# Performance work log

Measured on AMD Instinct MI355X. Metric: run time of the kernel, lower is better.

Reference implementation:

```python
import jax, jax.numpy as jnp
import numpy as np


def _pairwise_l2(x):
    # x: [N, D] -> [N, N] Euclidean distances, matching (x_i - x_j).norm(dim=-1)
    sq = jnp.sum(x * x, axis=-1)                      # [N]
    sqd = sq[:, None] + sq[None, :] - 2.0 * (x @ x.T)  # [N, N] squared distances
    sqd = jnp.maximum(sqd, 0.0)
    # safe sqrt: zero distance (diagonal) -> 0 with zero gradient, matching
    # torch's norm subgradient at 0
    pos = sqd > 0.0
    return jnp.where(pos, jnp.sqrt(jnp.where(pos, sqd, 1.0)), 0.0)


def setup_inputs() -> dict:
    key = jax.random.key(0)
    data = jax.random.normal(key, (8192, 256), dtype=jnp.float32)
    return {"data": data}


def reference(data) -> jnp.ndarray:
    x = data.reshape(data.shape[0], -1)               # [N, D]
    dist = _pairwise_l2(x)                            # [N, N]
    denom = jax.lax.stop_gradient(jnp.sum(dist, axis=1, keepdims=True))
    return dist / denom
```

## Files before the change

kernel.cpp:

```cpp
#include <hip/hip_runtime.h>
#include <stdint.h>

#define NN 8192
#define DD 256

typedef __attribute__((ext_vector_type(8))) short short8;
typedef __attribute__((ext_vector_type(4))) float f32x4;

typedef const uint32_t __attribute__((address_space(1)))* gbl_ptr_t;
typedef uint32_t __attribute__((address_space(3)))* lds_ptr_t;

__device__ __forceinline__ void gl_lds16(const void* g, const void* l) {
    __builtin_amdgcn_global_load_lds((gbl_ptr_t)(uintptr_t)g,
                                     (lds_ptr_t)(uintptr_t)l, 16, 0, 0);
}

__device__ __forceinline__ unsigned short f32_to_bf16(float f) {
    uint32_t u = __float_as_uint(f);
    u += 0x7fff + ((u >> 16) & 1);
    return (unsigned short)(u >> 16);
}
__device__ __forceinline__ float bf16_to_f32(unsigned short h) {
    return __uint_as_float(((uint32_t)h) << 16);
}

__global__ void prep_kernel(const float* __restrict__ x,
                            unsigned short* __restrict__ hi,
                            unsigned short* __restrict__ lo,
                            float* __restrict__ sq,
                            float* __restrict__ denom) {
    const int r = blockIdx.x;
    const int t = threadIdx.x;
    float v = x[(size_t)r * DD + t];
    unsigned short h = f32_to_bf16(v);
    unsigned short l = f32_to_bf16(v - bf16_to_f32(h));
    int csw = (t & ~63) | ((((t >> 3) & 7) ^ (r & 7)) << 3) | (t & 7);
    hi[(size_t)r * DD + csw] = h;
    lo[(size_t)r * DD + csw] = l;

    float s = v * v;
    #pragma unroll
    for (int m = 32; m >= 1; m >>= 1) s += __shfl_xor(s, m, 64);
    __shared__ float ws[4];
    if ((t & 63) == 0) ws[t >> 6] = s;
    __syncthreads();
    if (t == 0) {
        sq[r] = ws[0] + ws[1] + ws[2] + ws[3];
        denom[r] = 0.0f;
    }
}

#define DIST_KLOOP()                                                          \
    for (int kt = 0; kt < 4; ++kt) {                                          \
        _Pragma("unroll")                                                     \
        for (int c = 0; c < 4; ++c) {                                         \
            int lin  = c * 256 + tid;                                         \
            int row  = lin >> 3;                                              \
            int col8 = lin & 7;                                               \
            size_t goffA = (size_t)(row0 + row) * DD + kt * 64 + col8 * 8;    \
            size_t goffB = (size_t)(col0 + row) * DD + kt * 64 + col8 * 8;    \
            size_t lbyte = (size_t)(c * 256 + wid * 64) * 16;                 \
            gl_lds16(hi + goffA, (const char*)ldsAhi + lbyte);                \
            gl_lds16(lo + goffA, (const char*)ldsAlo + lbyte);                \
            gl_lds16(hi + goffB, (const char*)ldsBhi + lbyte);                \
            gl_lds16(lo + goffB, (const char*)ldsBlo + lbyte);                \
        }                                                                     \
        __syncthreads();                                                      \
        _Pragma("unroll")                                                     \
        for (int ks = 0; ks < 2; ++ks) {                                      \
            short8 ah[4], al[4], bh[4], bl[4];                                \
            _Pragma("unroll")                                                 \
            for (int fm = 0; fm < 4; ++fm) {                                  \
                int row = wm * 64 + fm * 16 + l15;                            \
                int cb  = (ks * 64 + lk * 16) ^ ((row & 7) << 4);             \
                int off = row * 64 + (cb >> 1);                               \
                ah[fm] = *(const short8*)(ldsAhi + off);                      \
                al[fm] = *(const short8*)(ldsAlo + off);                      \
            }                                                                 \
            _Pragma("unroll")                                                 \
            for (int fn = 0; fn < 4; ++fn) {                                  \
                int row = wn * 64 + fn * 16 + l15;                            \
                int cb  = (ks * 64 + lk * 16) ^ ((row & 7) << 4);             \
                int off = row * 64 + (cb >> 1);                               \
                bh[fn] = *(const short8*)(ldsBhi + off);                      \
                bl[fn] = *(const short8*)(ldsBlo + off);                      \
            }                                                                 \
            _Pragma("unroll")                                                 \
            for (int fm = 0; fm < 4; ++fm)                                    \
                _Pragma("unroll")                                             \
                for (int fn = 0; fn < 4; ++fn) {                              \
                    acc[fm][fn] = __builtin_amdgcn_mfma_f32_16x16x32_bf16(    \
                        ah[fm], bh[fn], acc[fm][fn], 0, 0, 0);                \
                    acc[fm][fn] = __builtin_amdgcn_mfma_f32_16x16x32_bf16(    \
                        ah[fm], bl[fn], acc[fm][fn], 0, 0, 0);                \
                    acc[fm][fn] = __builtin_amdgcn_mfma_f32_16x16x32_bf16(    \
                        al[fm], bh[fn], acc[fm][fn], 0, 0, 0);                \
                }                                                             \
        }                                                                     \
        __syncthreads();                                                      \
    }

#define DIST_PROLOG()                                                         \
    const int tid  = threadIdx.x;                                             \
    const int lane = tid & 63;                                                \
    const int wid  = tid >> 6;                                                \
    const int wm = wid >> 1, wn = wid & 1;                                    \
    const int l15 = lane & 15, lk = lane >> 4;                                \
    int t = blockIdx.x, bi = 0;                                               \
    while (t >= 64 - bi) { t -= 64 - bi; ++bi; }                              \
    const int bj = bi + t;                                                    \
    const int row0 = bi * 128;                                                \
    const int col0 = bj * 128;                                                \
    const bool offdiag = (bj > bi);                                           \
    f32x4 acc[4][4];                                                          \
    _Pragma("unroll")                                                         \
    for (int a = 0; a < 4; ++a)                                               \
        _Pragma("unroll")                                                     \
        for (int b = 0; b < 4; ++b) acc[a][b] = (f32x4){0.f, 0.f, 0.f, 0.f};  \
    float rsq[4][4], csq[4];                                                  \
    _Pragma("unroll")                                                         \
    for (int fm = 0; fm < 4; ++fm)                                            \
        _Pragma("unroll")                                                     \
        for (int r = 0; r < 4; ++r)                                           \
            rsq[fm][r] = sq[row0 + wm * 64 + fm * 16 + lk * 4 + r];           \
    _Pragma("unroll")                                                         \
    for (int fn = 0; fn < 4; ++fn)                                            \
        csq[fn] = sq[col0 + wn * 64 + fn * 16 + l15];

__launch_bounds__(256, 2)
__global__ void sum_kernel(const unsigned short* __restrict__ hi,
                           const unsigned short* __restrict__ lo,
                           const float* __restrict__ sq,
                           float* __restrict__ denom) {
    __shared__ __align__(16) unsigned short lds[4 * 128 * 64];
    unsigned short* ldsAhi = lds;
    unsigned short* ldsAlo = lds + 8192;
    unsigned short* ldsBhi = lds + 16384;
    unsigned short* ldsBlo = lds + 24576;

    DIST_PROLOG()
    DIST_KLOOP()

    float rp[4][4], cp[4];
    #pragma unroll
    for (int a = 0; a < 4; ++a) {
        cp[a] = 0.f;
        #pragma unroll
        for (int b = 0; b < 4; ++b) rp[a][b] = 0.f;
    }
    #pragma unroll
    for (int fm = 0; fm < 4; ++fm)
        #pragma unroll
        for (int fn = 0; fn < 4; ++fn)
            #pragma unroll
            for (int r = 0; r < 4; ++r) {
                float sqd = rsq[fm][r] + csq[fn] - 2.0f * acc[fm][fn][r];
                float d = sqrtf(fmaxf(sqd, 0.0f));
                rp[fm][r] += d;
                if (offdiag) cp[fn] += d;
            }

    #pragma unroll
    for (int fm = 0; fm < 4; ++fm)
        #pragma unroll
        for (int r = 0; r < 4; ++r) {
            float v = rp[fm][r];
            v += __shfl_xor(v, 1, 64);
            v += __shfl_xor(v, 2, 64);
            v += __shfl_xor(v, 4, 64);
            v += __shfl_xor(v, 8, 64);
            if (l15 == 0)
                atomicAdd(&denom[row0 + wm * 64 + fm * 16 + lk * 4 + r], v);
        }
    if (offdiag) {
        #pragma unroll
        for (int fn = 0; fn < 4; ++fn) {
            float v = cp[fn];
            v += __shfl_xor(v, 16, 64);
            v += __shfl_xor(v, 32, 64);
            if (lane < 16)
                atomicAdd(&denom[col0 + wn * 64 + fn * 16 + l15], v);
        }
    }
}

__global__ void inv_kernel(float* __restrict__ denom) {
    int i = blockIdx.x * 256 + threadIdx.x;
    if (i < NN) denom[i] = 1.0f / denom[i];
}

__launch_bounds__(256, 2)
__global__ void write_kernel(const unsigned short* __restrict__ hi,
                             const unsigned short* __restrict__ lo,
                             const float* __restrict__ sq,
                             const float* __restrict__ inv,
                             float* __restrict__ out) {
    __shared__ __align__(16) unsigned short lds[4 * 128 * 64];
    unsigned short* ldsAhi = lds;
    unsigned short* ldsAlo = lds + 8192;
    unsigned short* ldsBhi = lds + 16384;
    unsigned short* ldsBlo = lds + 24576;

    DIST_PROLOG()

    float rinv[4][4];
    #pragma unroll
    for (int fm = 0; fm < 4; ++fm)
        #pragma unroll
        for (int r = 0; r < 4; ++r)
            rinv[fm][r] = inv[row0 + wm * 64 + fm * 16 + lk * 4 + r];

    DIST_KLOOP()

    float* ldsT = reinterpret_cast<float*>(lds);

    #pragma unroll
    for (int fm = 0; fm < 4; ++fm)
        #pragma unroll
        for (int fn = 0; fn < 4; ++fn)
            #pragma unroll
            for (int r = 0; r < 4; ++r) {
                float sqd = rsq[fm][r] + csq[fn] - 2.0f * acc[fm][fn][r];
                float d = sqrtf(fmaxf(sqd, 0.0f));
                int lr = wm * 64 + fm * 16 + lk * 4 + r;
                int lc = wn * 64 + fn * 16 + l15;
                out[(size_t)(row0 + lr) * NN + col0 + lc] = d * rinv[fm][r];
                if (offdiag)
                    ldsT[lc * 128 + (lr ^ ((lc & 31) ^ ((lc & 4) << 2)))] = d;
            }

    if (offdiag) {
        __syncthreads();
        #pragma unroll
        for (int it = 0; it < 64; ++it) {
            int idx = it * 256 + tid;
            int c  = idx >> 7;
            int r_ = idx & 127;
            float d = ldsT[c * 128 + (r_ ^ ((c & 31) ^ ((c & 4) << 2)))];
            out[(size_t)(col0 + c) * NN + row0 + r_] = d * inv[col0 + c];
        }
    }
}

extern "C" void kernel_launch(void* const* d_in, const int* in_sizes, int n_in,
                              void* d_out, int out_size, void* d_ws, size_t ws_size,
                              hipStream_t stream) {
    const float* x = (const float*)d_in[0];
    float* out = (float*)d_out;
    char* ws = (char*)d_ws;
    unsigned short* hi = (unsigned short*)ws;
    unsigned short* lo = (unsigned short*)(ws + (size_t)NN * DD * 2);
    float* sq    = (float*)(ws + (size_t)NN * DD * 4);
    float* denom = (float*)(ws + (size_t)NN * DD * 4 + NN * 4);

    prep_kernel<<<NN, 256, 0, stream>>>(x, hi, lo, sq, denom);
    sum_kernel<<<2080, 256, 0, stream>>>(hi, lo, sq, denom);
    inv_kernel<<<32, 256, 0, stream>>>(denom);
    write_kernel<<<2080, 256, 0, stream>>>(hi, lo, sq, denom, out);
}
```

Before: 425.6 us.

## Double-buffer K-loop with async LDS prefetch and remap block-to-tile order

Replaces the single-buffered 4-step K loop (64-wide K tiles, loads then barrier) with an 8-step loop over 32-wide K tiles that alternates between two LDS buffers. The next-but-one stage's global-to-LDS loads are issued while the current stage computes, and explicit vmcnt/lgkmcnt waits and barriers control the hand-off. The XOR swizzle in the prep kernel and the LDS reads change to match the new 32-column tile layout. The block index is also permuted across groups of 8 to change which tiles run together, and a sync is added before the write kernel reuses LDS for the transpose. The hand-written waitcnt values are fragile and must exactly match the number of outstanding loads per stage.

```diff
diff --git a/kernel.cpp b/kernel.cpp
--- a/kernel.cpp
+++ b/kernel.cpp
@@ -23,6 +23,14 @@
 __device__ __forceinline__ float bf16_to_f32(unsigned short h) {
     return __uint_as_float(((uint32_t)h) << 16);
 }
+
+#define WAITVM8()  do { asm volatile("s_waitcnt vmcnt(8)" ::: "memory"); \
+                        __builtin_amdgcn_sched_barrier(0); } while (0)
+#define WAITVM0()  do { asm volatile("s_waitcnt vmcnt(0)" ::: "memory"); \
+                        __builtin_amdgcn_sched_barrier(0); } while (0)
+#define WAITLG0()  do { asm volatile("s_waitcnt lgkmcnt(0)" ::: "memory"); \
+                        __builtin_amdgcn_sched_barrier(0); } while (0)
+#define BAR()      __builtin_amdgcn_s_barrier()
 
 __global__ void prep_kernel(const float* __restrict__ x,
                             unsigned short* __restrict__ hi,
@@ -34,7 +42,7 @@
     float v = x[(size_t)r * DD + t];
     unsigned short h = f32_to_bf16(v);
     unsigned short l = f32_to_bf16(v - bf16_to_f32(h));
-    int csw = (t & ~63) | ((((t >> 3) & 7) ^ (r & 7)) << 3) | (t & 7);
+    int csw = (t & ~31) | ((((t >> 3) & 3) ^ (r & 3)) << 3) | (t & 7);
     hi[(size_t)r * DD + csw] = h;
     lo[(size_t)r * DD + csw] = l;
 
@@ -50,54 +58,62 @@
     }
 }
 
+#define STAGE(st, p) do {                                                     \
+    _Pragma("unroll")                                                         \
+    for (int c = 0; c < 2; ++c) {                                             \
+        int lin  = c * 256 + tid;                                             \
+        int row  = lin >> 2;                                                  \
+        int col8 = lin & 3;                                                   \
+        size_t gA = (size_t)(row0 + row) * DD + (st) * 32 + col8 * 8;         \
+        size_t gB = (size_t)(col0 + row) * DD + (st) * 32 + col8 * 8;         \
+        char* bse = (char*)lds + (p) * 32768 + (c * 256 + wid * 64) * 16;     \
+        gl_lds16(hi + gA, bse);                                               \
+        gl_lds16(lo + gA, bse + 8192);                                        \
+        gl_lds16(hi + gB, bse + 16384);                                       \
+        gl_lds16(lo + gB, bse + 24576);                                       \
+    } } while (0)
+
 #define DIST_KLOOP()                                                          \
-    for (int kt = 0; kt < 4; ++kt) {                                          \
-        _Pragma("unroll")                                                     \
-        for (int c = 0; c < 4; ++c) {                                         \
-            int lin  = c * 256 + tid;                                         \
-            int row  = lin >> 3;                                              \
-            int col8 = lin & 7;                                               \
-            size_t goffA = (size_t)(row0 + row) * DD + kt * 64 + col8 * 8;    \
-            size_t goffB = (size_t)(col0 + row) * DD + kt * 64 + col8 * 8;    \
-            size_t lbyte = (size_t)(c * 256 + wid * 64) * 16;                 \
-            gl_lds16(hi + goffA, (const char*)ldsAhi + lbyte);                \
-            gl_lds16(lo + goffA, (const char*)ldsAlo + lbyte);                \
-            gl_lds16(hi + goffB, (const char*)ldsBhi + lbyte);                \
-            gl_lds16(lo + goffB, (const char*)ldsBlo + lbyte);                \
+    STAGE(0, 0);                                                              \
+    STAGE(1, 1);                                                              \
+    WAITVM8(); BAR();                                                         \
+    _Pragma("unroll")                                                         \
+    for (int t = 0; t < 8; ++t) {                                             \
+        const int p = t & 1;                                                  \
+        unsigned short* L = lds + p * 16384;                                  \
+        short8 ah[4], al[4], bh[4], bl[4];                                    \
+        _Pragma("unroll")                                                     \
+        for (int fm = 0; fm < 4; ++fm) {                                      \
+            int row = wm * 64 + fm * 16 + l15;                                \
+            int cb  = (lk * 16) ^ ((row & 3) << 4);                           \
+            int off = row * 32 + (cb >> 1);                                   \
+            ah[fm] = *(const short8*)(L + off);                               \
+            al[fm] = *(const short8*)(L + 4096 + off);                        \
         }                                                                     \
-        __syncthreads();                                                      \
-        _Pragma("unroll")                                                     \
-        for (int ks = 0; ks < 2; ++ks) {                                      \
-            short8 ah[4], al[4], bh[4], bl[4];                                \
-            _Pragma("unroll")                                                 \
-            for (int fm = 0; fm < 4; ++fm) {                                  \
-                int row = wm * 64 + fm * 16 + l15;                            \
-                int cb  = (ks * 64 + lk * 16) ^ ((row & 7) << 4);             \
-                int off = row * 64 + (cb >> 1);                               \
-                ah[fm] = *(const short8*)(ldsAhi + off);                      \
-                al[fm] = *(const short8*)(ldsAlo + off);                      \
-            }                                                                 \
+        _Pragma("unroll")                                                     \
+        for (int fn = 0; fn < 4; ++fn) {                                      \
+            int row = wn * 64 + fn * 16 + l15;                                \
+            int cb  = (lk * 16) ^ ((row & 3) << 4);                           \
+            int off = row * 32 + (cb >> 1);                                   \
+            bh[fn] = *(const short8*)(L + 8192 + off);                        \
+            bl[fn] = *(const short8*)(L + 12288 + off);                       \
+        }                                                                     \
+        _Pragma("unroll")                                                     \
+        for (int fm = 0; fm < 4; ++fm)                                        \
             _Pragma("unroll")                                                 \
             for (int fn = 0; fn < 4; ++fn) {                                  \
-                int row = wn * 64 + fn * 16 + l15;                            \
-                int cb  = (ks * 64 + lk * 16) ^ ((row & 7) << 4);             \
-                int off = row * 64 + (cb >> 1);                               \
-                bh[fn] = *(const short8*)(ldsBhi + off);                      \
-                bl[fn] = *(const short8*)(ldsBlo + off);                      \
+                acc[fm][fn] = __builtin_amdgcn_mfma_f32_16x16x32_bf16(        \
+                    ah[fm], bh[fn], acc[fm][fn], 0, 0, 0);                    \
+                acc[fm][fn] = __builtin_amdgcn_mfma_f32_16x16x32_bf16(        \
+                    ah[fm], bl[fn], acc[fm][fn], 0, 0, 0);                    \
+                acc[fm][fn] = __builtin_amdgcn_mfma_f32_16x16x32_bf16(        \
+                    al[fm], bh[fn], acc[fm][fn], 0, 0, 0);                    \
             }                                                                 \
-            _Pragma("unroll")                                                 \
-            for (int fm = 0; fm < 4; ++fm)                                    \
-                _Pragma("unroll")                                             \
-                for (int fn = 0; fn < 4; ++fn) {                              \
-                    acc[fm][fn] = __builtin_amdgcn_mfma_f32_16x16x32_bf16(    \
-                        ah[fm], bh[fn], acc[fm][fn], 0, 0, 0);                \
-                    acc[fm][fn] = __builtin_amdgcn_mfma_f32_16x16x32_bf16(    \
-                        ah[fm], bl[fn], acc[fm][fn], 0, 0, 0);                \
-                    acc[fm][fn] = __builtin_amdgcn_mfma_f32_16x16x32_bf16(    \
-                        al[fm], bh[fn], acc[fm][fn], 0, 0, 0);                \
-                }                                                             \
-        }                                                                     \
-        __syncthreads();                                                      \
+        WAITLG0(); BAR();                  \
+        if (t + 2 < 8) STAGE(t + 2, p);               \
+        if (t < 6)      { WAITVM8(); }    \
+        else if (t == 6){ WAITVM0(); }                        \
+        if (t < 7) BAR();                      \
     }
 
 #define DIST_PROLOG()                                                         \
@@ -106,9 +122,11 @@
     const int wid  = tid >> 6;                                                \
     const int wm = wid >> 1, wn = wid & 1;                                    \
     const int l15 = lane & 15, lk = lane >> 4;                                \
-    int t = blockIdx.x, bi = 0;                                               \
-    while (t >= 64 - bi) { t -= 64 - bi; ++bi; }                              \
-    const int bj = bi + t;                                                    \
+           \
+    int wg = (blockIdx.x & 7) * 260 + (blockIdx.x >> 3);                      \
+    int t_ = wg, bi = 0;                                                      \
+    while (t_ >= 64 - bi) { t_ -= 64 - bi; ++bi; }                            \
+    const int bj = bi + t_;                                                   \
     const int row0 = bi * 128;                                                \
     const int col0 = bj * 128;                                                \
     const bool offdiag = (bj > bi);                                           \
@@ -132,12 +150,7 @@
                            const unsigned short* __restrict__ lo,
                            const float* __restrict__ sq,
                            float* __restrict__ denom) {
-    __shared__ __align__(16) unsigned short lds[4 * 128 * 64];
-    unsigned short* ldsAhi = lds;
-    unsigned short* ldsAlo = lds + 8192;
-    unsigned short* ldsBhi = lds + 16384;
-    unsigned short* ldsBlo = lds + 24576;
-
+    __shared__ __align__(16) unsigned short lds[2 * 16384];
     DIST_PROLOG()
     DIST_KLOOP()
 
@@ -195,12 +208,7 @@
                              const float* __restrict__ sq,
                              const float* __restrict__ inv,
                              float* __restrict__ out) {
-    __shared__ __align__(16) unsigned short lds[4 * 128 * 64];
-    unsigned short* ldsAhi = lds;
-    unsigned short* ldsAlo = lds + 8192;
-    unsigned short* ldsBhi = lds + 16384;
-    unsigned short* ldsBlo = lds + 24576;
-
+    __shared__ __align__(16) unsigned short lds[2 * 16384];
     DIST_PROLOG()
 
     float rinv[4][4];
@@ -212,6 +220,7 @@
 
     DIST_KLOOP()
 
+    __syncthreads();
     float* ldsT = reinterpret_cast<float*>(lds);
 
     #pragma unroll
```

New measurement: 427.6 us. No clear change (+0.4%).
